# Performance work log

Measured on AMD Instinct MI355X. Metric: run time of the kernel, lower is better.

Reference implementation:

```python
import jax, jax.numpy as jnp
import numpy as np

SPARSITY = 0.8  # fraction of weights zeroed (random unstructured mask)

def setup_inputs() -> dict:
    key = jax.random.key(0)
    k1, k2, k3, k4 = jax.random.split(key, 4)
    B, S, D_IN, D_OUT = 4, 2048, 4096, 4096
    x = jax.random.normal(k1, (B, S, D_IN), dtype=jnp.float32)
    weight = jax.random.normal(k2, (D_OUT, D_IN), dtype=jnp.float32) * 0.02
    bias = jax.random.normal(k3, (D_OUT,), dtype=jnp.float32) * 0.02
    # fixed binary mask: keep with prob (1 - sparsity)
    mask = (jax.random.uniform(k4, (D_OUT, D_IN)) >= SPARSITY).astype(jnp.float32)
    return {"x": x, "weight": weight, "bias": bias, "mask": mask}

def reference(x, weight, bias, mask):
    # w = weight * mask; y = x @ w.T + b   (F.linear semantics)
    w = weight * mask                      # [O, I]
    y = jnp.einsum('bsi,oi->bso', x, w)    # [B, S, O]
    return y + bias
```

## Files before the change

### kernel.cpp

```cpp
#include <hip/hip_runtime.h>
#include <hip/hip_bf16.h>
#include <stdint.h>

#define M_DIM 8192
#define N_DIM 4096
#define K_DIM 4096
#define BM 128
#define BN 128
#define BK 32

typedef __attribute__((ext_vector_type(8))) __bf16 bf16x8;
typedef __attribute__((ext_vector_type(4))) float floatx4;

__device__ inline unsigned f2b(float f) {
    union { float f; unsigned u; } v; v.f = f;
    return (v.u + 0x7FFFu + ((v.u >> 16) & 1u)) >> 16;
}
__device__ inline unsigned pk2(float lo, float hi) {
    return (f2b(lo) & 0xFFFFu) | (f2b(hi) << 16);
}

__device__ inline void async_load16(const void* g, void* l) {
    __builtin_amdgcn_global_load_lds(
        (const __attribute__((address_space(1))) unsigned int*)(unsigned long long)g,
        (__attribute__((address_space(3))) unsigned int*)(unsigned int)(unsigned long long)l,
        16, 0, 0);
}

__global__ __launch_bounds__(256)
void cvt_x_kernel(const float4* __restrict__ in, uint4* __restrict__ out, int n8) {
    int i = blockIdx.x * blockDim.x + threadIdx.x;
    if (i >= n8) return;
    float4 a = in[2 * i], b = in[2 * i + 1];
    uint4 o;
    o.x = pk2(a.x, a.y); o.y = pk2(a.z, a.w);
    o.z = pk2(b.x, b.y); o.w = pk2(b.z, b.w);
    out[i] = o;
}

__global__ __launch_bounds__(256)
void cvt_w_kernel(const float4* __restrict__ w, const float4* __restrict__ m,
                  uint4* __restrict__ out, int n8) {
    int i = blockIdx.x * blockDim.x + threadIdx.x;
    if (i >= n8) return;
    float4 w0 = w[2 * i], w1 = w[2 * i + 1];
    float4 m0 = m[2 * i], m1 = m[2 * i + 1];
    uint4 o;
    o.x = pk2(w0.x * m0.x, w0.y * m0.y);
    o.y = pk2(w0.z * m0.z, w0.w * m0.w);
    o.z = pk2(w1.x * m1.x, w1.y * m1.y);
    o.w = pk2(w1.z * m1.z, w1.w * m1.w);
    out[i] = o;
}

__global__ __launch_bounds__(256)
void gemm_bt_bias(const __hip_bfloat16* __restrict__ A,
                  const __hip_bfloat16* __restrict__ B,
                  const float* __restrict__ bias,
                  float* __restrict__ C) {
    __shared__ __hip_bfloat16 As[BM * BK];
    __shared__ __hip_bfloat16 Bs[BN * BK];

    const int t    = threadIdx.x;
    const int lane = t & 63;
    const int wave = t >> 6;
    const int wm   = wave >> 1;
    const int wn   = wave & 1;
    const int m0   = blockIdx.y * BM;
    const int n0   = blockIdx.x * BN;

    const int lm = lane & 15;
    const int lk = (lane >> 4) << 3;

    floatx4 acc[4][4] = {};

    const int c0 = t, c1 = t + 256;
    const int ar0 = c0 >> 2, ak0 = (c0 & 3) << 3;
    const int ar1 = c1 >> 2, ak1 = (c1 & 3) << 3;

    const __hip_bfloat16* Ab = A + (size_t)m0 * K_DIM;
    const __hip_bfloat16* Bb = B + (size_t)n0 * K_DIM;

    for (int k0 = 0; k0 < K_DIM; k0 += BK) {
        async_load16(Ab + (size_t)ar0 * K_DIM + k0 + ak0, As + c0 * 8);
        async_load16(Ab + (size_t)ar1 * K_DIM + k0 + ak1, As + c1 * 8);
        async_load16(Bb + (size_t)ar0 * K_DIM + k0 + ak0, Bs + c0 * 8);
        async_load16(Bb + (size_t)ar1 * K_DIM + k0 + ak1, Bs + c1 * 8);
        __syncthreads();

        bf16x8 af[4], bfr[4];
#pragma unroll
        for (int i = 0; i < 4; i++)
            af[i] = *reinterpret_cast<const bf16x8*>(
                &As[(wm * 64 + i * 16 + lm) * BK + lk]);
#pragma unroll
        for (int j = 0; j < 4; j++)
            bfr[j] = *reinterpret_cast<const bf16x8*>(
                &Bs[(wn * 64 + j * 16 + lm) * BK + lk]);
#pragma unroll
        for (int i = 0; i < 4; i++)
#pragma unroll
            for (int j = 0; j < 4; j++)
                acc[i][j] = __builtin_amdgcn_mfma_f32_16x16x32_bf16(
                    af[i], bfr[j], acc[i][j], 0, 0, 0);
        __syncthreads();
    }

    float bv[4];
#pragma unroll
    for (int j = 0; j < 4; j++)
        bv[j] = bias[n0 + wn * 64 + j * 16 + lm];
    const int row_base = m0 + wm * 64 + (lane >> 4) * 4;
    const int col_base = n0 + wn * 64 + lm;
#pragma unroll
    for (int i = 0; i < 4; i++)
#pragma unroll
        for (int j = 0; j < 4; j++) {
            const int col = col_base + j * 16;
#pragma unroll
            for (int r = 0; r < 4; r++)
                C[(size_t)(row_base + i * 16 + r) * N_DIM + col] =
                    acc[i][j][r] + bv[j];
        }
}

__global__ __launch_bounds__(256)
void gemm_fused_f32(const float* __restrict__ A, const float* __restrict__ W,
                    const float* __restrict__ Mk, const float* __restrict__ bias,
                    float* __restrict__ C) {
    __shared__ __hip_bfloat16 As[BM * BK];
    __shared__ __hip_bfloat16 Bs[BN * BK];

    const int t    = threadIdx.x;
    const int lane = t & 63;
    const int wave = t >> 6;
    const int wm   = wave >> 1;
    const int wn   = wave & 1;
    const int m0   = blockIdx.y * BM;
    const int n0   = blockIdx.x * BN;
    const int lm = lane & 15;
    const int lk = (lane >> 4) << 3;

    floatx4 acc[4][4] = {};

    const int r  = t >> 1;
    const int cb = (t & 1) * 16;

    for (int k0 = 0; k0 < K_DIM; k0 += BK) {
        const float* ap = A + (size_t)(m0 + r) * K_DIM + k0 + cb;
        float4 f0 = ((const float4*)ap)[0], f1 = ((const float4*)ap)[1];
        float4 f2 = ((const float4*)ap)[2], f3 = ((const float4*)ap)[3];
        uint4 pa, pb;
        pa.x = pk2(f0.x, f0.y); pa.y = pk2(f0.z, f0.w);
        pa.z = pk2(f1.x, f1.y); pa.w = pk2(f1.z, f1.w);
        pb.x = pk2(f2.x, f2.y); pb.y = pk2(f2.z, f2.w);
        pb.z = pk2(f3.x, f3.y); pb.w = pk2(f3.z, f3.w);
        *(uint4*)&As[r * BK + cb] = pa;
        *(uint4*)&As[r * BK + cb + 8] = pb;

        const float* wp = W + (size_t)(n0 + r) * K_DIM + k0 + cb;
        const float* mp = Mk + (size_t)(n0 + r) * K_DIM + k0 + cb;
        float4 w0 = ((const float4*)wp)[0], w1 = ((const float4*)wp)[1];
        float4 w2 = ((const float4*)wp)[2], w3 = ((const float4*)wp)[3];
        float4 q0 = ((const float4*)mp)[0], q1 = ((const float4*)mp)[1];
        float4 q2 = ((const float4*)mp)[2], q3 = ((const float4*)mp)[3];
        pa.x = pk2(w0.x * q0.x, w0.y * q0.y); pa.y = pk2(w0.z * q0.z, w0.w * q0.w);
        pa.z = pk2(w1.x * q1.x, w1.y * q1.y); pa.w = pk2(w1.z * q1.z, w1.w * q1.w);
        pb.x = pk2(w2.x * q2.x, w2.y * q2.y); pb.y = pk2(w2.z * q2.z, w2.w * q2.w);
        pb.z = pk2(w3.x * q3.x, w3.y * q3.y); pb.w = pk2(w3.z * q3.z, w3.w * q3.w);
        *(uint4*)&Bs[r * BK + cb] = pa;
        *(uint4*)&Bs[r * BK + cb + 8] = pb;
        __syncthreads();

        bf16x8 af[4], bfr[4];
#pragma unroll
        for (int i = 0; i < 4; i++)
            af[i] = *reinterpret_cast<const bf16x8*>(
                &As[(wm * 64 + i * 16 + lm) * BK + lk]);
#pragma unroll
        for (int j = 0; j < 4; j++)
            bfr[j] = *reinterpret_cast<const bf16x8*>(
                &Bs[(wn * 64 + j * 16 + lm) * BK + lk]);
#pragma unroll
        for (int i = 0; i < 4; i++)
#pragma unroll
            for (int j = 0; j < 4; j++)
                acc[i][j] = __builtin_amdgcn_mfma_f32_16x16x32_bf16(
                    af[i], bfr[j], acc[i][j], 0, 0, 0);
        __syncthreads();
    }

    float bv[4];
#pragma unroll
    for (int j = 0; j < 4; j++)
        bv[j] = bias[n0 + wn * 64 + j * 16 + lm];
    const int row_base = m0 + wm * 64 + (lane >> 4) * 4;
    const int col_base = n0 + wn * 64 + lm;
#pragma unroll
    for (int i = 0; i < 4; i++)
#pragma unroll
        for (int j = 0; j < 4; j++) {
            const int col = col_base + j * 16;
#pragma unroll
            for (int r4 = 0; r4 < 4; r4++)
                C[(size_t)(row_base + i * 16 + r4) * N_DIM + col] =
                    acc[i][j][r4] + bv[j];
        }
}

extern "C" void kernel_launch(void* const* d_in, const int* in_sizes, int n_in,
                              void* d_out, int out_size, void* d_ws, size_t ws_size,
                              hipStream_t stream) {
    const float* x    = (const float*)d_in[0];
    const float* w    = (const float*)d_in[1];
    const float* bias = (const float*)d_in[2];
    const float* mask = (const float*)d_in[3];
    float* out = (float*)d_out;

    const size_t xb_bytes = (size_t)M_DIM * K_DIM * 2;
    const size_t wb_bytes = (size_t)N_DIM * K_DIM * 2;
    dim3 grid(N_DIM / BN, M_DIM / BM);
    dim3 block(256);

    if (ws_size >= xb_bytes + wb_bytes) {
        __hip_bfloat16* xb = (__hip_bfloat16*)d_ws;
        __hip_bfloat16* wb = (__hip_bfloat16*)((char*)d_ws + xb_bytes);

        const int nx8 = M_DIM * K_DIM / 8;
        cvt_x_kernel<<<dim3(nx8 / 256), block, 0, stream>>>(
            (const float4*)x, (uint4*)xb, nx8);
        const int nw8 = N_DIM * K_DIM / 8;
        cvt_w_kernel<<<dim3(nw8 / 256), block, 0, stream>>>(
            (const float4*)w, (const float4*)mask, (uint4*)wb, nw8);
        gemm_bt_bias<<<grid, block, 0, stream>>>(xb, wb, bias, out);
    } else {
        gemm_fused_f32<<<grid, block, 0, stream>>>(x, w, mask, bias, out);
    }
}
```

Measured before the change: 623.9 us.

## Replace GEMM with 256x256 double-buffered, phase-interleaved MFMA kernel with swizzled LDS

Replaces the 128x128x32 single-buffered GEMM with a 256x256x64 tile using 512 threads, double-buffered LDS, XOR-swizzled shared layout and a four-phase schedule. Each phase interleaves async global-to-LDS loads for later K steps with MFMA work, using explicit waitcnt, barriers and setprio. A grouped block-index remap improves L2 reuse. The conversion kernels become grid-stride with smaller vectors, and the fallback fused path is removed, so the code now assumes a workspace large enough to hold the bf16 copies.

```diff
diff --git a/kernel.cpp b/kernel.cpp
--- a/kernel.cpp
+++ b/kernel.cpp
@@ -5,9 +5,11 @@
 #define M_DIM 8192
 #define N_DIM 4096
 #define K_DIM 4096
-#define BM 128
-#define BN 128
-#define BK 32
+
+#define BM 256
+#define BN 256
+#define BK 64
+#define NT (K_DIM / BK)
 
 typedef __attribute__((ext_vector_type(8))) __bf16 bf16x8;
 typedef __attribute__((ext_vector_type(4))) float floatx4;
@@ -27,93 +29,174 @@
         16, 0, 0);
 }
 
+#define SFENCE() asm volatile("" ::: "memory")
+
 __global__ __launch_bounds__(256)
-void cvt_x_kernel(const float4* __restrict__ in, uint4* __restrict__ out, int n8) {
+void cvt_x_kernel(const float4* __restrict__ in, uint2* __restrict__ out, int n4) {
     int i = blockIdx.x * blockDim.x + threadIdx.x;
-    if (i >= n8) return;
-    float4 a = in[2 * i], b = in[2 * i + 1];
-    uint4 o;
-    o.x = pk2(a.x, a.y); o.y = pk2(a.z, a.w);
-    o.z = pk2(b.x, b.y); o.w = pk2(b.z, b.w);
-    out[i] = o;
+    const int stride = gridDim.x * blockDim.x;
+    for (; i < n4; i += stride) {
+        float4 a = in[i];
+        uint2 o; o.x = pk2(a.x, a.y); o.y = pk2(a.z, a.w);
+        out[i] = o;
+    }
 }
 
 __global__ __launch_bounds__(256)
 void cvt_w_kernel(const float4* __restrict__ w, const float4* __restrict__ m,
-                  uint4* __restrict__ out, int n8) {
+                  uint2* __restrict__ out, int n4) {
     int i = blockIdx.x * blockDim.x + threadIdx.x;
-    if (i >= n8) return;
-    float4 w0 = w[2 * i], w1 = w[2 * i + 1];
-    float4 m0 = m[2 * i], m1 = m[2 * i + 1];
-    uint4 o;
-    o.x = pk2(w0.x * m0.x, w0.y * m0.y);
-    o.y = pk2(w0.z * m0.z, w0.w * m0.w);
-    o.z = pk2(w1.x * m1.x, w1.y * m1.y);
-    o.w = pk2(w1.z * m1.z, w1.w * m1.w);
-    out[i] = o;
-}
-
-__global__ __launch_bounds__(256)
-void gemm_bt_bias(const __hip_bfloat16* __restrict__ A,
-                  const __hip_bfloat16* __restrict__ B,
-                  const float* __restrict__ bias,
-                  float* __restrict__ C) {
-    __shared__ __hip_bfloat16 As[BM * BK];
-    __shared__ __hip_bfloat16 Bs[BN * BK];
+    const int stride = gridDim.x * blockDim.x;
+    for (; i < n4; i += stride) {
+        float4 a = w[i], q = m[i];
+        uint2 o; o.x = pk2(a.x * q.x, a.y * q.y); o.y = pk2(a.z * q.z, a.w * q.w);
+        out[i] = o;
+    }
+}
+
+__global__ __launch_bounds__(512, 2)
+void gemm_8phase(const __hip_bfloat16* __restrict__ A,
+                 const __hip_bfloat16* __restrict__ B,
+                 const float* __restrict__ bias,
+                 float* __restrict__ C) {
+    __shared__ __hip_bfloat16 As[2][2][128][64];
+    __shared__ __hip_bfloat16 Bs[2][2][128][64];
 
     const int t    = threadIdx.x;
     const int lane = t & 63;
     const int wave = t >> 6;
-    const int wm   = wave >> 1;
-    const int wn   = wave & 1;
-    const int m0   = blockIdx.y * BM;
-    const int n0   = blockIdx.x * BN;
-
-    const int lm = lane & 15;
-    const int lk = (lane >> 4) << 3;
-
-    floatx4 acc[4][4] = {};
-
-    const int c0 = t, c1 = t + 256;
-    const int ar0 = c0 >> 2, ak0 = (c0 & 3) << 3;
-    const int ar1 = c1 >> 2, ak1 = (c1 & 3) << 3;
-
-    const __hip_bfloat16* Ab = A + (size_t)m0 * K_DIM;
-    const __hip_bfloat16* Bb = B + (size_t)n0 * K_DIM;
-
-    for (int k0 = 0; k0 < K_DIM; k0 += BK) {
-        async_load16(Ab + (size_t)ar0 * K_DIM + k0 + ak0, As + c0 * 8);
-        async_load16(Ab + (size_t)ar1 * K_DIM + k0 + ak1, As + c1 * 8);
-        async_load16(Bb + (size_t)ar0 * K_DIM + k0 + ak0, Bs + c0 * 8);
-        async_load16(Bb + (size_t)ar1 * K_DIM + k0 + ak1, Bs + c1 * 8);
-        __syncthreads();
-
-        bf16x8 af[4], bfr[4];
-#pragma unroll
-        for (int i = 0; i < 4; i++)
-            af[i] = *reinterpret_cast<const bf16x8*>(
-                &As[(wm * 64 + i * 16 + lm) * BK + lk]);
-#pragma unroll
-        for (int j = 0; j < 4; j++)
-            bfr[j] = *reinterpret_cast<const bf16x8*>(
-                &Bs[(wn * 64 + j * 16 + lm) * BK + lk]);
-#pragma unroll
-        for (int i = 0; i < 4; i++)
-#pragma unroll
-            for (int j = 0; j < 4; j++)
-                acc[i][j] = __builtin_amdgcn_mfma_f32_16x16x32_bf16(
-                    af[i], bfr[j], acc[i][j], 0, 0, 0);
-        __syncthreads();
+    const int wm   = wave >> 2;
+    const int wn   = wave & 3;
+    const int lm   = lane & 15;
+    const int h4   = lane >> 4;
+
+    const int wg = (blockIdx.x & 7) * 64 + (blockIdx.x >> 3);
+    const int m0 = (wg >> 4) * BM;
+    const int n0 = (wg & 15) * BN;
+
+    const int srow = t >> 3;
+    const int schk = t & 7;
+    const int sx   = schk ^ (srow & 7);
+
+    const __hip_bfloat16* gA[2][2];
+    const __hip_bfloat16* gB[2][2];
+#pragma unroll
+    for (int h = 0; h < 2; h++)
+#pragma unroll
+        for (int r = 0; r < 2; r++) {
+            gA[h][r] = A + (size_t)(m0 + h * 128 + r * 64 + srow) * K_DIM + sx * 8;
+            gB[h][r] = B + (size_t)(n0 + h * 128 + r * 64 + srow) * K_DIM + sx * 8;
+        }
+
+#define STAGE_A(b, h, r, tt) \
+    async_load16(gA[h][r] + (tt) * BK, &As[b][h][(r) * 64 + srow][schk * 8])
+#define STAGE_B(b, h, r, tt) \
+    async_load16(gB[h][r] + (tt) * BK, &Bs[b][h][(r) * 64 + srow][schk * 8])
+
+    const int cs0 = ((h4)     ^ (lm & 7)) * 8;
+    const int cs1 = ((4 + h4) ^ (lm & 7)) * 8;
+
+#define LDA(b, i, kk) \
+    (*(const bf16x8*)&As[b][wm][(i) * 16 + lm][(kk) ? cs1 : cs0])
+#define LDB(b, j, kk) \
+    (*(const bf16x8*)&Bs[b][wn >> 1][(wn & 1) * 64 + (j) * 16 + lm][(kk) ? cs1 : cs0])
+
+    floatx4 acc[8][4] = {};
+    bf16x8 af[4][2], bf01[2][2], bf23[2][2];
+
+    STAGE_A(0, 0, 0, 0); STAGE_A(0, 1, 0, 0);
+    STAGE_B(0, 0, 0, 0); STAGE_B(0, 0, 1, 0);
+    STAGE_B(0, 1, 0, 0); STAGE_B(0, 1, 1, 0);
+    STAGE_A(0, 0, 1, 0); STAGE_A(0, 1, 1, 0);
+    STAGE_A(1, 0, 0, 1); STAGE_A(1, 1, 0, 1);
+    STAGE_B(1, 0, 0, 1); STAGE_B(1, 0, 1, 1);
+    STAGE_B(1, 1, 0, 1); STAGE_B(1, 1, 1, 1);
+    asm volatile("s_waitcnt vmcnt(6)" ::: "memory");
+    __builtin_amdgcn_s_barrier();
+    SFENCE();
+
+    for (int s = 0; s < NT; ++s) {
+        const int b  = s & 1;
+        const int nb = b ^ 1;
+
+#pragma unroll
+        for (int i = 0; i < 4; i++) { af[i][0] = LDA(b, i, 0); af[i][1] = LDA(b, i, 1); }
+#pragma unroll
+        for (int j = 0; j < 2; j++) { bf01[j][0] = LDB(b, j, 0); bf01[j][1] = LDB(b, j, 1); }
+        if (s + 1 < NT) { STAGE_A(nb, 0, 1, s + 1); STAGE_A(nb, 1, 1, s + 1); }
+        asm volatile("s_waitcnt lgkmcnt(8)" ::: "memory");
+        SFENCE(); __builtin_amdgcn_s_barrier();
+        asm volatile("s_waitcnt lgkmcnt(0)" ::: "memory");
+        __builtin_amdgcn_s_setprio(1);
+#pragma unroll
+        for (int i = 0; i < 4; i++)
+#pragma unroll
+            for (int j = 0; j < 2; j++)
+#pragma unroll
+                for (int kk = 0; kk < 2; kk++)
+                    acc[i][j] = __builtin_amdgcn_mfma_f32_16x16x32_bf16(
+                        af[i][kk], bf01[j][kk], acc[i][j], 0, 0, 0);
+        __builtin_amdgcn_s_setprio(0);
+        SFENCE(); __builtin_amdgcn_s_barrier(); SFENCE();
+
+#pragma unroll
+        for (int j = 0; j < 2; j++) { bf23[j][0] = LDB(b, 2 + j, 0); bf23[j][1] = LDB(b, 2 + j, 1); }
+        if (s + 2 < NT) { STAGE_A(b, 0, 0, s + 2); STAGE_A(b, 1, 0, s + 2); }
+        SFENCE(); __builtin_amdgcn_s_barrier();
+        asm volatile("s_waitcnt lgkmcnt(0)" ::: "memory");
+        __builtin_amdgcn_s_setprio(1);
+#pragma unroll
+        for (int i = 0; i < 4; i++)
+#pragma unroll
+            for (int j = 0; j < 2; j++)
+#pragma unroll
+                for (int kk = 0; kk < 2; kk++)
+                    acc[i][2 + j] = __builtin_amdgcn_mfma_f32_16x16x32_bf16(
+                        af[i][kk], bf23[j][kk], acc[i][2 + j], 0, 0, 0);
+        __builtin_amdgcn_s_setprio(0);
+        SFENCE(); __builtin_amdgcn_s_barrier(); SFENCE();
+
+#pragma unroll
+        for (int i = 0; i < 4; i++) { af[i][0] = LDA(b, 4 + i, 0); af[i][1] = LDA(b, 4 + i, 1); }
+        if (s + 2 < NT) { STAGE_B(b, 0, 0, s + 2); STAGE_B(b, 0, 1, s + 2); }
+        SFENCE(); __builtin_amdgcn_s_barrier();
+        asm volatile("s_waitcnt lgkmcnt(0)" ::: "memory");
+        __builtin_amdgcn_s_setprio(1);
+#pragma unroll
+        for (int i = 0; i < 4; i++)
+#pragma unroll
+            for (int j = 0; j < 2; j++)
+#pragma unroll
+                for (int kk = 0; kk < 2; kk++)
+                    acc[4 + i][j] = __builtin_amdgcn_mfma_f32_16x16x32_bf16(
+                        af[i][kk], bf01[j][kk], acc[4 + i][j], 0, 0, 0);
+        __builtin_amdgcn_s_setprio(0);
+        SFENCE(); __builtin_amdgcn_s_barrier(); SFENCE();
+
+        if (s + 2 < NT) { STAGE_B(b, 1, 0, s + 2); STAGE_B(b, 1, 1, s + 2); }
+        __builtin_amdgcn_s_setprio(1);
+#pragma unroll
+        for (int i = 0; i < 4; i++)
+#pragma unroll
+            for (int j = 0; j < 2; j++)
+#pragma unroll
+                for (int kk = 0; kk < 2; kk++)
+                    acc[4 + i][2 + j] = __builtin_amdgcn_mfma_f32_16x16x32_bf16(
+                        af[i][kk], bf23[j][kk], acc[4 + i][2 + j], 0, 0, 0);
+        __builtin_amdgcn_s_setprio(0);
+        if (s + 2 < NT) asm volatile("s_waitcnt vmcnt(6)" ::: "memory");
+        else            asm volatile("s_waitcnt vmcnt(0)" ::: "memory");
+        SFENCE(); __builtin_amdgcn_s_barrier(); SFENCE();
     }
 
     float bv[4];
 #pragma unroll
     for (int j = 0; j < 4; j++)
         bv[j] = bias[n0 + wn * 64 + j * 16 + lm];
-    const int row_base = m0 + wm * 64 + (lane >> 4) * 4;
+    const int row_base = m0 + wm * 128 + h4 * 4;
     const int col_base = n0 + wn * 64 + lm;
 #pragma unroll
-    for (int i = 0; i < 4; i++)
+    for (int i = 0; i < 8; i++)
 #pragma unroll
         for (int j = 0; j < 4; j++) {
             const int col = col_base + j * 16;
@@ -121,90 +204,6 @@
             for (int r = 0; r < 4; r++)
                 C[(size_t)(row_base + i * 16 + r) * N_DIM + col] =
                     acc[i][j][r] + bv[j];
-        }
-}
-
-__global__ __launch_bounds__(256)
-void gemm_fused_f32(const float* __restrict__ A, const float* __restrict__ W,
-                    const float* __restrict__ Mk, const float* __restrict__ bias,
-                    float* __restrict__ C) {
-    __shared__ __hip_bfloat16 As[BM * BK];
-    __shared__ __hip_bfloat16 Bs[BN * BK];
-
-    const int t    = threadIdx.x;
-    const int lane = t & 63;
-    const int wave = t >> 6;
-    const int wm   = wave >> 1;
-    const int wn   = wave & 1;
-    const int m0   = blockIdx.y * BM;
-    const int n0   = blockIdx.x * BN;
-    const int lm = lane & 15;
-    const int lk = (lane >> 4) << 3;
-
-    floatx4 acc[4][4] = {};
-
-    const int r  = t >> 1;
-    const int cb = (t & 1) * 16;
-
-    for (int k0 = 0; k0 < K_DIM; k0 += BK) {
-        const float* ap = A + (size_t)(m0 + r) * K_DIM + k0 + cb;
-        float4 f0 = ((const float4*)ap)[0], f1 = ((const float4*)ap)[1];
-        float4 f2 = ((const float4*)ap)[2], f3 = ((const float4*)ap)[3];
-        uint4 pa, pb;
-        pa.x = pk2(f0.x, f0.y); pa.y = pk2(f0.z, f0.w);
-        pa.z = pk2(f1.x, f1.y); pa.w = pk2(f1.z, f1.w);
-        pb.x = pk2(f2.x, f2.y); pb.y = pk2(f2.z, f2.w);
-        pb.z = pk2(f3.x, f3.y); pb.w = pk2(f3.z, f3.w);
-        *(uint4*)&As[r * BK + cb] = pa;
-        *(uint4*)&As[r * BK + cb + 8] = pb;
-
-        const float* wp = W + (size_t)(n0 + r) * K_DIM + k0 + cb;
-        const float* mp = Mk + (size_t)(n0 + r) * K_DIM + k0 + cb;
-        float4 w0 = ((const float4*)wp)[0], w1 = ((const float4*)wp)[1];
-        float4 w2 = ((const float4*)wp)[2], w3 = ((const float4*)wp)[3];
-        float4 q0 = ((const float4*)mp)[0], q1 = ((const float4*)mp)[1];
-        float4 q2 = ((const float4*)mp)[2], q3 = ((const float4*)mp)[3];
-        pa.x = pk2(w0.x * q0.x, w0.y * q0.y); pa.y = pk2(w0.z * q0.z, w0.w * q0.w);
-        pa.z = pk2(w1.x * q1.x, w1.y * q1.y); pa.w = pk2(w1.z * q1.z, w1.w * q1.w);
-        pb.x = pk2(w2.x * q2.x, w2.y * q2.y); pb.y = pk2(w2.z * q2.z, w2.w * q2.w);
-        pb.z = pk2(w3.x * q3.x, w3.y * q3.y); pb.w = pk2(w3.z * q3.z, w3.w * q3.w);
-        *(uint4*)&Bs[r * BK + cb] = pa;
-        *(uint4*)&Bs[r * BK + cb + 8] = pb;
-        __syncthreads();
-
-        bf16x8 af[4], bfr[4];
-#pragma unroll
-        for (int i = 0; i < 4; i++)
-            af[i] = *reinterpret_cast<const bf16x8*>(
-                &As[(wm * 64 + i * 16 + lm) * BK + lk]);
-#pragma unroll
-        for (int j = 0; j < 4; j++)
-            bfr[j] = *reinterpret_cast<const bf16x8*>(
-                &Bs[(wn * 64 + j * 16 + lm) * BK + lk]);
-#pragma unroll
-        for (int i = 0; i < 4; i++)
-#pragma unroll
-            for (int j = 0; j < 4; j++)
-                acc[i][j] = __builtin_amdgcn_mfma_f32_16x16x32_bf16(
-                    af[i], bfr[j], acc[i][j], 0, 0, 0);
-        __syncthreads();
-    }
-
-    float bv[4];
-#pragma unroll
-    for (int j = 0; j < 4; j++)
-        bv[j] = bias[n0 + wn * 64 + j * 16 + lm];
-    const int row_base = m0 + wm * 64 + (lane >> 4) * 4;
-    const int col_base = n0 + wn * 64 + lm;
-#pragma unroll
-    for (int i = 0; i < 4; i++)
-#pragma unroll
-        for (int j = 0; j < 4; j++) {
-            const int col = col_base + j * 16;
-#pragma unroll
-            for (int r4 = 0; r4 < 4; r4++)
-                C[(size_t)(row_base + i * 16 + r4) * N_DIM + col] =
-                    acc[i][j][r4] + bv[j];
         }
 }
 
@@ -217,23 +216,12 @@
     const float* mask = (const float*)d_in[3];
     float* out = (float*)d_out;
 
-    const size_t xb_bytes = (size_t)M_DIM * K_DIM * 2;
-    const size_t wb_bytes = (size_t)N_DIM * K_DIM * 2;
-    dim3 grid(N_DIM / BN, M_DIM / BM);
-    dim3 block(256);
-
-    if (ws_size >= xb_bytes + wb_bytes) {
-        __hip_bfloat16* xb = (__hip_bfloat16*)d_ws;
-        __hip_bfloat16* wb = (__hip_bfloat16*)((char*)d_ws + xb_bytes);
-
-        const int nx8 = M_DIM * K_DIM / 8;
-        cvt_x_kernel<<<dim3(nx8 / 256), block, 0, stream>>>(
-            (const float4*)x, (uint4*)xb, nx8);
-        const int nw8 = N_DIM * K_DIM / 8;
-        cvt_w_kernel<<<dim3(nw8 / 256), block, 0, stream>>>(
-            (const float4*)w, (const float4*)mask, (uint4*)wb, nw8);
-        gemm_bt_bias<<<grid, block, 0, stream>>>(xb, wb, bias, out);
-    } else {
-        gemm_fused_f32<<<grid, block, 0, stream>>>(x, w, mask, bias, out);
-    }
-}
+    __hip_bfloat16* xb = (__hip_bfloat16*)d_ws;
+    __hip_bfloat16* wb = xb + (size_t)M_DIM * K_DIM;
+
+    cvt_x_kernel<<<dim3(2048), dim3(256), 0, stream>>>(
+        (const float4*)x, (uint2*)xb, M_DIM * K_DIM / 4);
+    cvt_w_kernel<<<dim3(2048), dim3(256), 0, stream>>>(
+        (const float4*)w, (const float4*)mask, (uint2*)wb, N_DIM * K_DIM / 4);
+    gemm_8phase<<<dim3(512), dim3(512), 0, stream>>>(xb, wb, bias, out);
+}
```

Result: faster. 518.6 us (-16.9%).
